# Performance work log

Hardware: AMD Instinct MI355X
Metric: run time of the kernel (lower is better)

The kernel has to match this reference:

```python
import jax, jax.numpy as jnp
import numpy as np

B = 256      # batch
ZD = 128     # z_dim
HIN = 128    # H_inputs
H = 512      # hidden
HT = 32      # H_t
N = 16384    # num nodes
RW = 16      # rw_len
TEMP = 1.0
P_DROP = 0.2
EPS_C = 0.1  # constraints epsilon


def setup_inputs() -> dict:
    key = jax.random.key(0)
    ks = jax.random.split(key, 20)
    def w(k, shape, fan):
        return (jax.random.normal(k, shape, jnp.float32) / np.float32(np.sqrt(fan)))
    z = lambda n: jnp.zeros((n,), jnp.float32)
    u = jax.random.uniform(ks[14], (RW, B, N), jnp.float32)
    return {
        "latent": jax.random.normal(ks[0], (B, ZD + 1), jnp.float32),
        "inputs0": jnp.zeros((B, HIN), jnp.float32),
        "Wc": w(ks[1], (ZD, ZD + 1), ZD + 1), "bc": z(ZD),
        "Ws": w(ks[2], (H, ZD), ZD), "bs": z(H),
        "Wh": w(ks[3], (H, H), H), "bh": z(H),
        "Wcc": w(ks[4], (H, H), H), "bcc": z(H),
        "W_ih": w(ks[5], (4 * H, HIN), HIN), "b_ih": z(4 * H),
        "W_hh": w(ks[6], (4 * H, H), H), "b_hh": z(4 * H),
        "W_up": w(ks[7], (N, H), H), "b_up": z(N),
        "W_down": w(ks[8], (HIN, N), N),
        "Wt_down": w(ks[9], (HT, H), H), "bt_down": z(HT),
        "Wt_pred": w(ks[10], (1, HT), HT),
        "Wt_up": w(ks[11], (HT, 1), 1), "bt_up": z(HT),
        "W_vt": w(ks[12], (HIN, HIN + HT), HIN + HT),
        "W_prob": w(ks[13], (1, HIN), HIN),
        # pre-sampled Gumbel noise per step (torch.rand -> gumbel)
        "gumbel": -jnp.log(-jnp.log(u + 1e-20) + 1e-20),
        # uniforms for dropout masks in TimeDecoder (forced train mode)
        "drop_u": jax.random.uniform(ks[15], (RW, B, HT), jnp.float32),
    }


def reference(latent, inputs0, Wc, bc, Ws, bs, Wh, bh, Wcc, bcc,
              W_ih, b_ih, W_hh, b_hh, W_up, b_up, W_down,
              Wt_down, bt_down, Wt_pred, Wt_up, bt_up, W_vt, W_prob,
              gumbel, drop_u):
    # induced=True path: compress latent, init (h, c)
    lat = jnp.tanh(latent @ Wc.T + bc)               # [B, ZD]
    s = jnp.tanh(lat @ Ws.T + bs)                    # [B, H]
    h0 = jnp.tanh(s @ Wh.T + bh)
    c0 = jnp.tanh(s @ Wcc.T + bcc)
    keep = 1.0 - P_DROP

    def step(carry, xs):
        x, h, c, last_t = carry
        g, du = xs
        # torch LSTMCell: gate order i, f, g, o
        gates = x @ W_ih.T + b_ih + h @ W_hh.T + b_hh  # [B, 4H]
        i, f, gg, o = jnp.split(gates, 4, axis=1)
        c2 = jax.nn.sigmoid(f) * c + jax.nn.sigmoid(i) * jnp.tanh(gg)
        h2 = jax.nn.sigmoid(o) * jnp.tanh(c2)
        # node logits + gumbel-softmax sample
        p = h2 @ W_up.T + b_up                         # [B, N]
        v = jax.nn.softmax((p + g) / TEMP, axis=1)
        Hg = v @ W_down.T                              # [B, HIN]
        # TimeDecoder (dropout always in train mode)
        td = jnp.tanh(h2 @ Wt_down.T + bt_down)        # [B, HT]
        td = td * (du < keep).astype(td.dtype) / keep
        t = jnp.minimum(td @ Wt_pred.T, 1.0)           # [B, 1]
        # constraints(t, last_t)
        mn = jnp.min(t)
        t = jnp.where(mn < EPS_C, t - mn, t)
        mx = jnp.max(t)
        t = jnp.where(mx > 1.0, t / mx, t)
        t = jnp.clip(t, last_t, 1.0)
        Ht = t @ Wt_up.T + bt_up                       # [B, HT]
        x2 = jnp.concatenate([Hg, Ht], axis=1) @ W_vt.T  # [B, HIN]
        return (x2, h2, c2, t), (v, t)

    last_t0 = jnp.zeros((latent.shape[0], 1), latent.dtype)
    (xf, _, _, _), (rw, ts) = jax.lax.scan(step, (inputs0, h0, c0, last_t0), (gumbel, drop_u))
    rw = jnp.transpose(rw, (1, 0, 2))   # [B, RW, N]
    ts = jnp.transpose(ts, (1, 0, 2))   # [B, RW, 1]
    prob = xf @ W_prob.T                # [B, 1]
    return rw, ts, prob
```

## Files before the change

kernel.cpp:

```cpp
#include <hip/hip_runtime.h>

typedef float  __attribute__((ext_vector_type(4))) f32x4;
typedef int    __attribute__((ext_vector_type(4))) i32x4;
typedef unsigned short u16;
typedef unsigned long long u64;

#define B    256
#define H    512
#define HIN  128
#define N    16384
#define RW   16
#define HT   32
#define KC2  672
#define RWN  262144
#define TS_OFF   67108864
#define PROB_OFF 67112960

__device__ __forceinline__ u16 f2bf(float f) {
  unsigned u = __builtin_bit_cast(unsigned, f);
  u += 0x7FFFu + ((u >> 16) & 1u);
  return (u16)(u >> 16);
}
__device__ __forceinline__ float bf2f(u16 v) {
  return __builtin_bit_cast(float, ((unsigned)v) << 16);
}
__device__ __forceinline__ float sigm(float x) { return 1.0f / (1.0f + expf(-x)); }

__device__ __forceinline__ void mfma(f32x4& d, i32x4 a, i32x4 b) {
  asm volatile("v_mfma_f32_16x16x32_bf16 %0, %1, %2, %0" : "+v"(d) : "v"(a), "v"(b));
}
__device__ __forceinline__ void mfma_n(f32x4& d, i32x4 a, i32x4 b) {
  asm volatile("s_nop 1\n\tv_mfma_f32_16x16x32_bf16 %0, %1, %2, %0" : "+v"(d) : "v"(a), "v"(b));
}
__device__ __forceinline__ void fence_acc(f32x4& v) {
  asm volatile("s_nop 7\n\ts_nop 7" : "+v"(v));
}

__global__ __launch_bounds__(256) void k_prep(
    const float* __restrict__ W_up, const float* __restrict__ W_down,
    const float* __restrict__ W_hh, const float* __restrict__ Wt_down,
    const float* __restrict__ b_ih, const float* __restrict__ b_hh,
    const float* __restrict__ Wh, const float* __restrict__ Wcc,
    u16* __restrict__ Wup_b, u16* __restrict__ Wdn_b, u16* __restrict__ Wfull,
    u16* __restrict__ Wtd_b, u16* __restrict__ Whc_b,
    float* __restrict__ bcomb, float* __restrict__ tstep, float* __restrict__ rowLs)
{
  const int idx0 = blockIdx.x * 256 + threadIdx.x;
  const int stride = gridDim.x * 256;
  for (int i = idx0; i < N * H; i += stride) Wup_b[i] = f2bf(W_up[i]);
  for (int i = idx0; i < HIN * N; i += stride) Wdn_b[i] = f2bf(W_down[i]);
  for (int i = idx0; i < 4 * H * H; i += stride) {
    int j = i >> 9, k = i & 511;
    Wfull[j * KC2 + 160 + k] = f2bf(W_hh[i]);
  }
  for (int i = idx0; i < HT * H; i += stride) Wtd_b[i] = f2bf(Wt_down[i]);
  for (int i = idx0; i < 2 * H * H; i += stride) {
    int j = i >> 9, k = i & 511;
    Whc_b[i] = f2bf(j < H ? Wh[j * H + k] : Wcc[(j - H) * H + k]);
  }
  for (int i = idx0; i < 4 * H; i += stride) bcomb[i] = b_ih[i] + b_hh[i];
  for (int i = idx0; i < B; i += stride) tstep[i] = 0.0f;
  for (int i = idx0; i < 16 * B; i += stride) rowLs[i] = 0.0f;
}

__global__ __launch_bounds__(256) void k_fold(
    const float* __restrict__ W_ih, const float* __restrict__ W_vt,
    const float* __restrict__ inputs0, const float* __restrict__ W_prob,
    u16* __restrict__ Wfull, float* __restrict__ g0add, float* __restrict__ wpc)
{
  int idx = blockIdx.x * 256 + threadIdx.x;
  if (idx < 2048 * 160) {
    int j = idx / 160, m = idx - j * 160;
    float a = 0.0f;
    for (int c = 0; c < HIN; ++c) a += W_ih[j * HIN + c] * W_vt[c * 160 + m];
    Wfull[j * KC2 + m] = f2bf(a);
  } else if (idx < 2048 * 160 + 256 * 2048) {
    int i2 = idx - 2048 * 160;
    int b = i2 >> 11, j = i2 & 2047;
    float a = 0.0f;
    for (int k = 0; k < HIN; ++k) a += inputs0[b * HIN + k] * W_ih[j * HIN + k];
    g0add[i2] = a;
  } else if (idx < 2048 * 160 + 256 * 2048 + 160) {
    int m = idx - (2048 * 160 + 256 * 2048);
    float a = 0.0f;
    for (int k = 0; k < HIN; ++k) a += W_prob[k] * W_vt[k * 160 + m];
    wpc[m] = a;
  }
}

__global__ __launch_bounds__(256) void k_lat(
    const float* __restrict__ latent, const float* __restrict__ Wc,
    const float* __restrict__ bc, float* __restrict__ latbuf)
{
  int idx = blockIdx.x * 256 + threadIdx.x;
  int b = idx >> 7, i = idx & 127;
  float acc = bc[i];
  for (int k = 0; k < 129; ++k) acc += latent[b * 129 + k] * Wc[i * 129 + k];
  latbuf[idx] = tanhf(acc);
}

__global__ __launch_bounds__(256) void k_sinit(
    const float* __restrict__ latbuf, const float* __restrict__ Ws,
    const float* __restrict__ bs, u16* __restrict__ sinit_b)
{
  int idx = blockIdx.x * 256 + threadIdx.x;
  int b = idx >> 9, j = idx & 511;
  float acc = bs[j];
  for (int k = 0; k < HIN; ++k) acc += latbuf[b * HIN + k] * Ws[j * HIN + k];
  sinit_b[idx] = f2bf(tanhf(acc));
}

__global__ __launch_bounds__(256) void k_h0c0m(
    const u16* __restrict__ sinit_b, const u16* __restrict__ Whc_b,
    const float* __restrict__ bh, const float* __restrict__ bcc,
    float* __restrict__ cbuf, u16* __restrict__ h0out)
{
  const int rb = blockIdx.x >> 6, cb = blockIdx.x & 63;
  const int wave = threadIdx.x >> 6, lane = threadIdx.x & 63;
  const int lr = lane & 15, lk = lane >> 4;
  const int m0 = rb * 16, col0 = cb * 16;
  const u16* ab = sinit_b + (m0 + lr) * H + wave * 128 + 8 * lk;
  const u16* bb = Whc_b + (col0 + lr) * H + wave * 128 + 8 * lk;
  f32x4 acc[2] = {};
  mfma_n(acc[0], *(const i32x4*)(ab),      *(const i32x4*)(bb));
  mfma_n(acc[1], *(const i32x4*)(ab + 32), *(const i32x4*)(bb + 32));
  mfma(acc[0], *(const i32x4*)(ab + 64), *(const i32x4*)(bb + 64));
  mfma(acc[1], *(const i32x4*)(ab + 96), *(const i32x4*)(bb + 96));
  fence_acc(acc[0]); fence_acc(acc[1]);
  __shared__ float q[4][16][17];
  #pragma unroll
  for (int rr = 0; rr < 4; ++rr)
    q[wave][4 * lk + rr][lr] = acc[0][rr] + acc[1][rr];
  __syncthreads();
  const int r2 = threadIdx.x >> 4, jj = threadIdx.x & 15;
  float s = q[0][r2][jj] + q[1][r2][jj] + q[2][r2][jj] + q[3][r2][jj];
  int col = col0 + jj;
  if (col < H) h0out[(m0 + r2) * H + col] = f2bf(tanhf(s + bh[col]));
  else         cbuf[(m0 + r2) * H + col - H] = tanhf(s + bcc[col - H]);
}

__global__ __launch_bounds__(256) void k_lstm2(
    const u16* __restrict__ hprev, u16* __restrict__ hcur,
    const u16* __restrict__ Wfull, const float* __restrict__ bcomb,
    float* __restrict__ cbuf, const float* __restrict__ g0,
    const u16* __restrict__ HgPart, const float* __restrict__ rowLs,
    const float* __restrict__ t0buf, float* __restrict__ tstep,
    const float* __restrict__ Wt_up, const float* __restrict__ bt_up,
    float* __restrict__ out, const u16* __restrict__ ebp, int r)
{
  const int blk = blockIdx.x, tid = threadIdx.x;
  const int wave = tid >> 6, lane = tid & 63;
  const int lr = lane & 15, lk = lane >> 4;
  const int rb = ((blk & 7) << 1) | ((blk >> 3) & 1);
  const int cb = blk >> 4;
  const int m0 = rb * 16, j0 = cb * 16;
  const float* rowLprev = rowLs + (r - 1) * B;

  __shared__ u16 aT[16][168];
  __shared__ float q[4][16][17];
  __shared__ float redS[8];
  __shared__ float tl[256];

  float tv = 0.0f;
  if (r > 0) {
    tv = t0buf[tid];
    float v = tv;
    #pragma unroll
    for (int off = 1; off < 64; off <<= 1) v = fminf(v, __shfl_xor(v, off));
    if (lane == 0) redS[wave] = v;
  }
  __syncthreads();
  if (r > 0) {
    float mn = fminf(fminf(redS[0], redS[1]), fminf(redS[2], redS[3]));
    if (mn < 0.1f) tv -= mn;
    float v = tv;
    #pragma unroll
    for (int off = 1; off < 64; off <<= 1) v = fmaxf(v, __shfl_xor(v, off));
    if (lane == 0) redS[4 + wave] = v;
  }
  __syncthreads();
  if (r > 0) {
    float mx = fmaxf(fmaxf(redS[4], redS[5]), fmaxf(redS[6], redS[7]));
    if (mx > 1.0f) tv /= mx;
    tv = fminf(fmaxf(tv, tstep[(r - 1) * B + tid]), 1.0f);
    if (blk == 0) {
      tstep[r * B + tid] = tv;
      out[TS_OFF + tid * RW + (r - 1)] = tv;
    }
  }
  tl[tid] = tv;

  {
    const int row = tid >> 4, c8 = (tid & 15) * 8;
    if (r > 0) {
      float s0 = 0.f, s1 = 0.f, s2 = 0.f, s3 = 0.f;
      float s4 = 0.f, s5 = 0.f, s6 = 0.f, s7 = 0.f;
      const u16* hp = HgPart + (size_t)(m0 + row) * HIN + c8;
      #pragma unroll 4
      for (int c = 0; c < 128; ++c) {
        i32x4 pk = *(const i32x4*)(hp + (size_t)c * (B * HIN));
        s0 += bf2f((u16)pk[0]); s1 += bf2f((u16)(pk[0] >> 16));
        s2 += bf2f((u16)pk[1]); s3 += bf2f((u16)(pk[1] >> 16));
        s4 += bf2f((u16)pk[2]); s5 += bf2f((u16)(pk[2] >> 16));
        s6 += bf2f((u16)pk[3]); s7 += bf2f((u16)(pk[3] >> 16));
      }
      float R = 1.0f / rowLprev[m0 + row];
      aT[row][c8 + 0] = f2bf(s0 * R); aT[row][c8 + 1] = f2bf(s1 * R);
      aT[row][c8 + 2] = f2bf(s2 * R); aT[row][c8 + 3] = f2bf(s3 * R);
      aT[row][c8 + 4] = f2bf(s4 * R); aT[row][c8 + 5] = f2bf(s5 * R);
      aT[row][c8 + 6] = f2bf(s6 * R); aT[row][c8 + 7] = f2bf(s7 * R);
    } else {
      #pragma unroll
      for (int e = 0; e < 8; ++e) aT[row][c8 + e] = 0;
    }
  }
  __syncthreads();

  for (int i2 = tid; i2 < 512; i2 += 256) {
    int row = i2 >> 5, j = i2 & 31;
    aT[row][128 + j] = (r > 0) ? f2bf(tl[m0 + row] * Wt_up[j] + bt_up[j]) : (u16)0;
  }

  if (r > 0) {
    #pragma unroll
    for (int uu = 0; uu < 8; ++uu) {
      int flat = (blk * 2048 + uu * 256 + tid) * 4;
      int row = flat >> 14;
      float Rv = 1.0f / rowLprev[row];
      u64 ev = *(const u64*)(ebp + flat);
      f32x4 o;
      o[0] = bf2f((u16)ev) * Rv;
      o[1] = bf2f((u16)(ev >> 16)) * Rv;
      o[2] = bf2f((u16)(ev >> 32)) * Rv;
      o[3] = bf2f((u16)(ev >> 48)) * Rv;
      *(f32x4*)(out + (size_t)row * RWN + (size_t)(r - 1) * N + (flat & (N - 1))) = o;
    }
  }
  __syncthreads();

  const int gcol = wave * H + j0 + lr;
  f32x4 acc[2] = {};
  const u16* brow = Wfull + (size_t)gcol * KC2 + 8 * lk;
  const u16* aL   = &aT[lr][8 * lk];
  const u16* arow = hprev + (m0 + lr) * H + 8 * lk;
  mfma_n(acc[0], *(const i32x4*)(aL),       *(const i32x4*)(brow));
  mfma_n(acc[1], *(const i32x4*)(aL + 32),  *(const i32x4*)(brow + 32));
  mfma(acc[0], *(const i32x4*)(aL + 64),  *(const i32x4*)(brow + 64));
  mfma(acc[1], *(const i32x4*)(aL + 96),  *(const i32x4*)(brow + 96));
  mfma(acc[0], *(const i32x4*)(aL + 128), *(const i32x4*)(brow + 128));
  #pragma unroll 4
  for (int i = 5; i < 21; ++i) {
    int kk = i * 32;
    mfma(acc[i & 1], *(const i32x4*)(arow + kk - 160), *(const i32x4*)(brow + kk));
  }
  fence_acc(acc[0]); fence_acc(acc[1]);
  float bias = bcomb[gcol];
  #pragma unroll
  for (int rr = 0; rr < 4; ++rr)
    q[wave][4 * lk + rr][lr] = acc[0][rr] + acc[1][rr] + bias;
  __syncthreads();
  const int r2 = tid >> 4, jj = tid & 15;
  const int b = m0 + r2, j = j0 + jj;
  float gi = q[0][r2][jj], gf = q[1][r2][jj], gg = q[2][r2][jj], go = q[3][r2][jj];
  if (r == 0) {
    const float* gp = g0 + b * 2048 + j;
    gi += gp[0]; gf += gp[512]; gg += gp[1024]; go += gp[1536];
  }
  float c  = cbuf[b * H + j];
  float c2 = sigm(gf) * c + sigm(gi) * tanhf(gg);
  float h2 = sigm(go) * tanhf(c2);
  cbuf[b * H + j] = c2;
  hcur[b * H + j] = f2bf(h2);
}

__global__ __launch_bounds__(256) void k_pgemm2(
    const u16* __restrict__ hb, const u16* __restrict__ Wup,
    const float* __restrict__ b_up, const float* __restrict__ gum,
    u16* __restrict__ eb, float* __restrict__ rowL,
    u16* __restrict__ HgPart, const u16* __restrict__ Wdn,
    const u16* __restrict__ Wtd, const float* __restrict__ bt_down,
    const float* __restrict__ Wt_pred, const float* __restrict__ du,
    float* __restrict__ t0)
{
  const int rb = blockIdx.x >> 7, cb = blockIdx.x & 127;
  const int wave = threadIdx.x >> 6, lane = threadIdx.x & 63;
  const int lr = lane & 15, lk = lane >> 4;
  const int m0 = rb * 32;
  const int n0 = cb * 128 + wave * 32;

  float gv[2][4][2], bup0 = b_up[n0 + lr], bup1 = b_up[n0 + 16 + lr];
  #pragma unroll
  for (int mi = 0; mi < 2; ++mi)
    #pragma unroll
    for (int rr = 0; rr < 4; ++rr) {
      int row = m0 + 16 * mi + 4 * lk + rr;
      gv[mi][rr][0] = gum[(size_t)row * N + n0 + lr];
      gv[mi][rr][1] = gum[(size_t)row * N + n0 + 16 + lr];
    }

  f32x4 acc[2][2] = {};
  const u16* a0 = hb + (m0 + lr) * H + 8 * lk;
  const u16* a1 = a0 + 16 * H;
  const u16* b0 = Wup + (size_t)(n0 + lr) * H + 8 * lk;
  const u16* b1 = b0 + 16 * H;
  {
    i32x4 af0 = *(const i32x4*)(a0);
    i32x4 af1 = *(const i32x4*)(a1);
    i32x4 bf0 = *(const i32x4*)(b0);
    i32x4 bf1 = *(const i32x4*)(b1);
    mfma_n(acc[0][0], af0, bf0); mfma_n(acc[0][1], af0, bf1);
    mfma_n(acc[1][0], af1, bf0); mfma_n(acc[1][1], af1, bf1);
  }
  #pragma unroll 3
  for (int kk = 32; kk < H; kk += 32) {
    i32x4 af0 = *(const i32x4*)(a0 + kk);
    i32x4 af1 = *(const i32x4*)(a1 + kk);
    i32x4 bf0 = *(const i32x4*)(b0 + kk);
    i32x4 bf1 = *(const i32x4*)(b1 + kk);
    mfma(acc[0][0], af0, bf0); mfma(acc[0][1], af0, bf1);
    mfma(acc[1][0], af1, bf0); mfma(acc[1][1], af1, bf1);
  }
  #pragma unroll
  for (int mi = 0; mi < 2; ++mi) { fence_acc(acc[mi][0]); fence_acc(acc[mi][1]); }

  __shared__ float eL[32][132];
  __shared__ float sL[4][32];
  #pragma unroll
  for (int mi = 0; mi < 2; ++mi)
    #pragma unroll
    for (int rr = 0; rr < 4; ++rr) {
      int rl = 16 * mi + 4 * lk + rr;
      int row = m0 + rl;
      u16* sp = eb + (size_t)row * N + n0 + lr;
      float v0 = acc[mi][0][rr] + bup0 + gv[mi][rr][0];
      float v1 = acc[mi][1][rr] + bup1 + gv[mi][rr][1];
      float e0 = expf(fminf(v0, 80.0f));
      float e1 = expf(fminf(v1, 80.0f));
      sp[0] = f2bf(e0); sp[16] = f2bf(e1);
      eL[rl][wave * 32 + lr] = e0;
      eL[rl][wave * 32 + 16 + lr] = e1;
      float par = e0 + e1;
      #pragma unroll
      for (int off = 1; off < 16; off <<= 1) par += __shfl_xor(par, off);
      if (lr == 0) sL[wave][rl] = par;
    }
  __syncthreads();
  if (threadIdx.x < 32)
    atomicAdd(rowL + m0 + threadIdx.x,
              sL[0][threadIdx.x] + sL[1][threadIdx.x] + sL[2][threadIdx.x] + sL[3][threadIdx.x]);

  const int nb = cb * 128;
  f32x4 acc2[2][2] = {};
  #pragma unroll
  for (int kk2 = 0; kk2 < 4; ++kk2) {
    i32x4 af[2];
    #pragma unroll
    for (int mi2 = 0; mi2 < 2; ++mi2) {
      const float* ep = &eL[16 * mi2 + lr][kk2 * 32 + 8 * lk];
      f32x4 x0 = *(const f32x4*)ep;
      f32x4 x1 = *(const f32x4*)(ep + 4);
      af[mi2][0] = (int)f2bf(x0[0]) | ((int)f2bf(x0[1]) << 16);
      af[mi2][1] = (int)f2bf(x0[2]) | ((int)f2bf(x0[3]) << 16);
      af[mi2][2] = (int)f2bf(x1[0]) | ((int)f2bf(x1[1]) << 16);
      af[mi2][3] = (int)f2bf(x1[2]) | ((int)f2bf(x1[3]) << 16);
    }
    i32x4 bf0 = *(const i32x4*)(Wdn + (size_t)(wave * 32 + lr) * N + nb + kk2 * 32 + 8 * lk);
    i32x4 bf1 = *(const i32x4*)(Wdn + (size_t)(wave * 32 + 16 + lr) * N + nb + kk2 * 32 + 8 * lk);
    mfma_n(acc2[0][0], af[0], bf0); mfma_n(acc2[0][1], af[0], bf1);
    mfma_n(acc2[1][0], af[1], bf0); mfma_n(acc2[1][1], af[1], bf1);
  }
  #pragma unroll
  for (int mi2 = 0; mi2 < 2; ++mi2) { fence_acc(acc2[mi2][0]); fence_acc(acc2[mi2][1]); }
  u16* hp = HgPart + (size_t)cb * (B * HIN);
  #pragma unroll
  for (int mi2 = 0; mi2 < 2; ++mi2)
    #pragma unroll
    for (int ni = 0; ni < 2; ++ni)
      #pragma unroll
      for (int rr = 0; rr < 4; ++rr)
        hp[(m0 + 16 * mi2 + 4 * lk + rr) * HIN + wave * 32 + 16 * ni + lr] =
            f2bf(acc2[mi2][ni][rr]);

  if (cb == 0 && wave < 2) {
    f32x4 acc3[2] = {};
    const u16* at = hb + (m0 + wave * 16 + lr) * H + 8 * lk;
    {
      i32x4 af = *(const i32x4*)(at);
      mfma_n(acc3[0], af, *(const i32x4*)(Wtd + lr * H + 8 * lk));
      mfma_n(acc3[1], af, *(const i32x4*)(Wtd + (16 + lr) * H + 8 * lk));
    }
    for (int kk = 32; kk < H; kk += 32) {
      i32x4 af = *(const i32x4*)(at + kk);
      mfma(acc3[0], af, *(const i32x4*)(Wtd + lr * H + kk + 8 * lk));
      mfma(acc3[1], af, *(const i32x4*)(Wtd + (16 + lr) * H + kk + 8 * lk));
    }
    fence_acc(acc3[0]); fence_acc(acc3[1]);
    float wp0 = Wt_pred[lr],  wp1 = Wt_pred[16 + lr];
    float bt0 = bt_down[lr],  bt1 = bt_down[16 + lr];
    #pragma unroll
    for (int rr = 0; rr < 4; ++rr) {
      int row = m0 + wave * 16 + 4 * lk + rr;
      float td0 = tanhf(acc3[0][rr] + bt0);
      float td1 = tanhf(acc3[1][rr] + bt1);
      td0 = (du[row * HT + lr]      < 0.8f) ? td0 * 1.25f : 0.0f;
      td1 = (du[row * HT + 16 + lr] < 0.8f) ? td1 * 1.25f : 0.0f;
      float part = td0 * wp0 + td1 * wp1;
      #pragma unroll
      for (int off = 1; off < 16; off <<= 1) part += __shfl_xor(part, off);
      if (lr == 0) t0[row] = fminf(part, 1.0f);
    }
  }
}

__global__ __launch_bounds__(256) void k_tail(
    float* __restrict__ out, const u16* __restrict__ eb15,
    const float* __restrict__ rowLs, const u16* __restrict__ HgPart,
    const float* __restrict__ t0buf, float* __restrict__ tstep,
    float* __restrict__ Hgf)
{
  const int blk = blockIdx.x, tid = threadIdx.x;
  const float* rowL15 = rowLs + 15 * B;
  #pragma unroll
  for (int uu = 0; uu < 4; ++uu) {
    int flat = (blk * 1024 + uu * 256 + tid) * 4;
    int row = flat >> 14;
    float Rv = 1.0f / rowL15[row];
    u64 ev = *(const u64*)(eb15 + flat);
    f32x4 o;
    o[0] = bf2f((u16)ev) * Rv;
    o[1] = bf2f((u16)(ev >> 16)) * Rv;
    o[2] = bf2f((u16)(ev >> 32)) * Rv;
    o[3] = bf2f((u16)(ev >> 48)) * Rv;
    *(f32x4*)(out + (size_t)row * RWN + (size_t)15 * N + (flat & (N - 1))) = o;
  }
  if (blk < 16) {
    const int row = blk * 16 + (tid >> 4), c8 = (tid & 15) * 8;
    float s[8] = {};
    const u16* hp = HgPart + (size_t)row * HIN + c8;
    #pragma unroll 4
    for (int c = 0; c < 128; ++c) {
      i32x4 pk = *(const i32x4*)(hp + (size_t)c * (B * HIN));
      s[0] += bf2f((u16)pk[0]); s[1] += bf2f((u16)(pk[0] >> 16));
      s[2] += bf2f((u16)pk[1]); s[3] += bf2f((u16)(pk[1] >> 16));
      s[4] += bf2f((u16)pk[2]); s[5] += bf2f((u16)(pk[2] >> 16));
      s[6] += bf2f((u16)pk[3]); s[7] += bf2f((u16)(pk[3] >> 16));
    }
    float R = 1.0f / rowL15[row];
    #pragma unroll
    for (int e = 0; e < 8; ++e) Hgf[row * HIN + c8 + e] = s[e] * R;
  }
  if (blk == 16) {
    const int wave = tid >> 6, lane = tid & 63;
    __shared__ float redS[8];
    float tv = t0buf[tid];
    float v = tv;
    #pragma unroll
    for (int off = 1; off < 64; off <<= 1) v = fminf(v, __shfl_xor(v, off));
    if (lane == 0) redS[wave] = v;
    __syncthreads();
    float mn = fminf(fminf(redS[0], redS[1]), fminf(redS[2], redS[3]));
    if (mn < 0.1f) tv -= mn;
    v = tv;
    #pragma unroll
    for (int off = 1; off < 64; off <<= 1) v = fmaxf(v, __shfl_xor(v, off));
    if (lane == 0) redS[4 + wave] = v;
    __syncthreads();
    float mx = fmaxf(fmaxf(redS[4], redS[5]), fmaxf(redS[6], redS[7]));
    if (mx > 1.0f) tv /= mx;
    tv = fminf(fmaxf(tv, tstep[15 * B + tid]), 1.0f);
    tstep[16 * B + tid] = tv;
    out[TS_OFF + tid * RW + 15] = tv;
  }
}

__global__ __launch_bounds__(256) void k_prob(
    const float* __restrict__ Hgf, const float* __restrict__ tstep,
    const float* __restrict__ Wt_up, const float* __restrict__ bt_up,
    const float* __restrict__ wpc, float* __restrict__ outp)
{
  int b = threadIdx.x;
  float acc = 0.0f;
  for (int m = 0; m < HIN; ++m) acc += Hgf[b * HIN + m] * wpc[m];
  float tv = tstep[16 * B + b];
  for (int j = 0; j < HT; ++j) acc += (tv * Wt_up[j] + bt_up[j]) * wpc[HIN + j];
  outp[b] = acc;
}

extern "C" void kernel_launch(void* const* d_in, const int* in_sizes, int n_in,
                              void* d_out, int out_size, void* d_ws, size_t ws_size,
                              hipStream_t stream) {
  (void)in_sizes; (void)n_in; (void)out_size; (void)ws_size;
  const float* latent  = (const float*)d_in[0];
  const float* inputs0 = (const float*)d_in[1];
  const float* Wc      = (const float*)d_in[2];
  const float* bc      = (const float*)d_in[3];
  const float* Ws      = (const float*)d_in[4];
  const float* bs      = (const float*)d_in[5];
  const float* Wh      = (const float*)d_in[6];
  const float* bh      = (const float*)d_in[7];
  const float* Wcc     = (const float*)d_in[8];
  const float* bcc     = (const float*)d_in[9];
  const float* W_ih    = (const float*)d_in[10];
  const float* b_ih    = (const float*)d_in[11];
  const float* W_hh    = (const float*)d_in[12];
  const float* b_hh    = (const float*)d_in[13];
  const float* W_up    = (const float*)d_in[14];
  const float* b_up    = (const float*)d_in[15];
  const float* W_down  = (const float*)d_in[16];
  const float* Wt_down = (const float*)d_in[17];
  const float* bt_down = (const float*)d_in[18];
  const float* Wt_pred = (const float*)d_in[19];
  const float* Wt_up   = (const float*)d_in[20];
  const float* bt_up   = (const float*)d_in[21];
  const float* W_vt    = (const float*)d_in[22];
  const float* W_prob  = (const float*)d_in[23];
  const float* gumbel  = (const float*)d_in[24];
  const float* drop_u  = (const float*)d_in[25];
  float* out = (float*)d_out;

  char* p = (char*)d_ws;
  auto alloc = [&](size_t bytes) { char* r = p; p += (bytes + 255) & ~(size_t)255; return r; };
  u16*   Wup_b  = (u16*)  alloc((size_t)N * H * 2);
  u16*   Wdn_b  = (u16*)  alloc((size_t)HIN * N * 2);
  u16*   Wfull_b= (u16*)  alloc((size_t)4 * H * KC2 * 2);
  u16*   Wtd_b  = (u16*)  alloc((size_t)HT * H * 2);
  u16*   Whc_b  = (u16*)  alloc((size_t)2 * H * H * 2);
  float* bcomb  = (float*)alloc(4 * H * 4);
  u16*   hbuf0  = (u16*)  alloc((size_t)B * H * 2);
  u16*   hbuf1  = (u16*)  alloc((size_t)B * H * 2);
  float* cbuf   = (float*)alloc((size_t)B * H * 4);
  u16*   sinit_b= (u16*)  alloc((size_t)B * H * 2);
  float* latbuf = (float*)alloc((size_t)B * HIN * 4);
  float* rowLs  = (float*)alloc((size_t)16 * B * 4);
  float* t0buf  = (float*)alloc(B * 4);
  float* tstep  = (float*)alloc((size_t)17 * B * 4);
  u16*   HgPart = (u16*)  alloc((size_t)128 * B * HIN * 2);
  float* Hgf    = (float*)alloc((size_t)B * HIN * 4);
  float* g0add  = (float*)alloc((size_t)B * 4 * H * 4);
  float* wpc    = (float*)alloc(160 * 4);
  u16*   ebuf0  = (u16*)  alloc((size_t)B * N * 2);
  u16*   ebuf1  = (u16*)  alloc((size_t)B * N * 2);

  k_prep<<<2048, 256, 0, stream>>>(W_up, W_down, W_hh, Wt_down, b_ih, b_hh, Wh, Wcc,
                                   Wup_b, Wdn_b, Wfull_b, Wtd_b, Whc_b, bcomb,
                                   tstep, rowLs);
  k_fold<<<3330, 256, 0, stream>>>(W_ih, W_vt, inputs0, W_prob, Wfull_b, g0add, wpc);
  k_lat  <<<128, 256, 0, stream>>>(latent, Wc, bc, latbuf);
  k_sinit<<<512, 256, 0, stream>>>(latbuf, Ws, bs, sinit_b);
  k_h0c0m<<<1024, 256, 0, stream>>>(sinit_b, Whc_b, bh, bcc, cbuf, hbuf1);

  for (int r = 0; r < 16; ++r) {
    u16* hprev = (r & 1) ? hbuf0 : hbuf1;
    u16* hcur  = (r & 1) ? hbuf1 : hbuf0;
    u16* eb    = (r & 1) ? ebuf1 : ebuf0;
    u16* ebp   = (r & 1) ? ebuf0 : ebuf1;
    k_lstm2<<<512, 256, 0, stream>>>(hprev, hcur, Wfull_b, bcomb, cbuf, g0add,
                                     HgPart, rowLs, t0buf, tstep, Wt_up, bt_up,
                                     out, ebp, r);
    k_pgemm2<<<1024, 256, 0, stream>>>(hcur, Wup_b, b_up, gumbel + (size_t)r * B * N,
                                       eb, rowLs + r * B, HgPart, Wdn_b,
                                       Wtd_b, bt_down, Wt_pred,
                                       drop_u + (size_t)r * B * HT, t0buf);
  }
  k_tail<<<1024, 256, 0, stream>>>(out, ebuf1, rowLs, HgPart, t0buf, tstep, Hgf);
  k_prob<<<1, 256, 0, stream>>>(Hgf, tstep, Wt_up, bt_up, wpc, out + PROB_OFF);
}
```

Measured before the change: 1.401 ms.

## Replace per-column-block Hg partial buffer with fp32 atomic accumulation

k_pgemm2 previously wrote 128 bf16 partial Hg tiles that k_lstm2 and k_tail then summed by reading 128 slices per element. The change accumulates the partials directly into a double-buffered fp32 Hg array with atomicAdd. The next k_lstm2 zeroes the other buffer and reads the finished sum with a single vector load. This removes the large partial-buffer traffic and the reduction loops, but adds heavy atomic contention: 128 column blocks add into each element. Summation order also becomes nondeterministic. The row-block mapping in k_lstm2 is simplified as well.

```diff
diff --git a/kernel.cpp b/kernel.cpp
--- a/kernel.cpp
+++ b/kernel.cpp
@@ -143,16 +143,16 @@
     const u16* __restrict__ hprev, u16* __restrict__ hcur,
     const u16* __restrict__ Wfull, const float* __restrict__ bcomb,
     float* __restrict__ cbuf, const float* __restrict__ g0,
-    const u16* __restrict__ HgPart, const float* __restrict__ rowLs,
-    const float* __restrict__ t0buf, float* __restrict__ tstep,
-    const float* __restrict__ Wt_up, const float* __restrict__ bt_up,
-    float* __restrict__ out, const u16* __restrict__ ebp, int r)
+    const float* __restrict__ HgfPrev, float* __restrict__ HgfNext,
+    const float* __restrict__ rowLs, const float* __restrict__ t0buf,
+    float* __restrict__ tstep, const float* __restrict__ Wt_up,
+    const float* __restrict__ bt_up, float* __restrict__ out,
+    const u16* __restrict__ ebp, int r)
 {
   const int blk = blockIdx.x, tid = threadIdx.x;
   const int wave = tid >> 6, lane = tid & 63;
   const int lr = lane & 15, lk = lane >> 4;
-  const int rb = ((blk & 7) << 1) | ((blk >> 3) & 1);
-  const int cb = blk >> 4;
+  const int rb = blk & 15, cb = blk >> 4;
   const int m0 = rb * 16, j0 = cb * 16;
   const float* rowLprev = rowLs + (r - 1) * B;
 
@@ -160,6 +160,8 @@
   __shared__ float q[4][16][17];
   __shared__ float redS[8];
   __shared__ float tl[256];
+
+  if (blk < 128) HgfNext[blk * 256 + tid] = 0.0f;
 
   float tv = 0.0f;
   if (r > 0) {
@@ -193,29 +195,21 @@
   {
     const int row = tid >> 4, c8 = (tid & 15) * 8;
     if (r > 0) {
-      float s0 = 0.f, s1 = 0.f, s2 = 0.f, s3 = 0.f;
-      float s4 = 0.f, s5 = 0.f, s6 = 0.f, s7 = 0.f;
-      const u16* hp = HgPart + (size_t)(m0 + row) * HIN + c8;
-      #pragma unroll 4
-      for (int c = 0; c < 128; ++c) {
-        i32x4 pk = *(const i32x4*)(hp + (size_t)c * (B * HIN));
-        s0 += bf2f((u16)pk[0]); s1 += bf2f((u16)(pk[0] >> 16));
-        s2 += bf2f((u16)pk[1]); s3 += bf2f((u16)(pk[1] >> 16));
-        s4 += bf2f((u16)pk[2]); s5 += bf2f((u16)(pk[2] >> 16));
-        s6 += bf2f((u16)pk[3]); s7 += bf2f((u16)(pk[3] >> 16));
-      }
+      const float* hp = HgfPrev + (m0 + row) * HIN + c8;
+      f32x4 x0 = *(const f32x4*)hp;
+      f32x4 x1 = *(const f32x4*)(hp + 4);
       float R = 1.0f / rowLprev[m0 + row];
-      aT[row][c8 + 0] = f2bf(s0 * R); aT[row][c8 + 1] = f2bf(s1 * R);
-      aT[row][c8 + 2] = f2bf(s2 * R); aT[row][c8 + 3] = f2bf(s3 * R);
-      aT[row][c8 + 4] = f2bf(s4 * R); aT[row][c8 + 5] = f2bf(s5 * R);
-      aT[row][c8 + 6] = f2bf(s6 * R); aT[row][c8 + 7] = f2bf(s7 * R);
+      aT[row][c8 + 0] = f2bf(x0[0] * R); aT[row][c8 + 1] = f2bf(x0[1] * R);
+      aT[row][c8 + 2] = f2bf(x0[2] * R); aT[row][c8 + 3] = f2bf(x0[3] * R);
+      aT[row][c8 + 4] = f2bf(x1[0] * R); aT[row][c8 + 5] = f2bf(x1[1] * R);
+      aT[row][c8 + 6] = f2bf(x1[2] * R); aT[row][c8 + 7] = f2bf(x1[3] * R);
     } else {
       #pragma unroll
       for (int e = 0; e < 8; ++e) aT[row][c8 + e] = 0;
     }
   }
-  __syncthreads();
-
+
+  __syncthreads();
   for (int i2 = tid; i2 < 512; i2 += 256) {
     int row = i2 >> 5, j = i2 & 31;
     aT[row][128 + j] = (r > 0) ? f2bf(tl[m0 + row] * Wt_up[j] + bt_up[j]) : (u16)0;
@@ -277,7 +271,7 @@
     const u16* __restrict__ hb, const u16* __restrict__ Wup,
     const float* __restrict__ b_up, const float* __restrict__ gum,
     u16* __restrict__ eb, float* __restrict__ rowL,
-    u16* __restrict__ HgPart, const u16* __restrict__ Wdn,
+    float* __restrict__ HgfAcc, const u16* __restrict__ Wdn,
     const u16* __restrict__ Wtd, const float* __restrict__ bt_down,
     const float* __restrict__ Wt_pred, const float* __restrict__ du,
     float* __restrict__ t0)
@@ -371,15 +365,14 @@
   }
   #pragma unroll
   for (int mi2 = 0; mi2 < 2; ++mi2) { fence_acc(acc2[mi2][0]); fence_acc(acc2[mi2][1]); }
-  u16* hp = HgPart + (size_t)cb * (B * HIN);
   #pragma unroll
   for (int mi2 = 0; mi2 < 2; ++mi2)
     #pragma unroll
     for (int ni = 0; ni < 2; ++ni)
       #pragma unroll
       for (int rr = 0; rr < 4; ++rr)
-        hp[(m0 + 16 * mi2 + 4 * lk + rr) * HIN + wave * 32 + 16 * ni + lr] =
-            f2bf(acc2[mi2][ni][rr]);
+        atomicAdd(HgfAcc + (m0 + 16 * mi2 + 4 * lk + rr) * HIN + wave * 32 + 16 * ni + lr,
+                  acc2[mi2][ni][rr]);
 
   if (cb == 0 && wave < 2) {
     f32x4 acc3[2] = {};
@@ -414,9 +407,8 @@
 
 __global__ __launch_bounds__(256) void k_tail(
     float* __restrict__ out, const u16* __restrict__ eb15,
-    const float* __restrict__ rowLs, const u16* __restrict__ HgPart,
-    const float* __restrict__ t0buf, float* __restrict__ tstep,
-    float* __restrict__ Hgf)
+    const float* __restrict__ rowLs, const float* __restrict__ t0buf,
+    float* __restrict__ tstep)
 {
   const int blk = blockIdx.x, tid = threadIdx.x;
   const float* rowL15 = rowLs + 15 * B;
@@ -433,23 +425,7 @@
     o[3] = bf2f((u16)(ev >> 48)) * Rv;
     *(f32x4*)(out + (size_t)row * RWN + (size_t)15 * N + (flat & (N - 1))) = o;
   }
-  if (blk < 16) {
-    const int row = blk * 16 + (tid >> 4), c8 = (tid & 15) * 8;
-    float s[8] = {};
-    const u16* hp = HgPart + (size_t)row * HIN + c8;
-    #pragma unroll 4
-    for (int c = 0; c < 128; ++c) {
-      i32x4 pk = *(const i32x4*)(hp + (size_t)c * (B * HIN));
-      s[0] += bf2f((u16)pk[0]); s[1] += bf2f((u16)(pk[0] >> 16));
-      s[2] += bf2f((u16)pk[1]); s[3] += bf2f((u16)(pk[1] >> 16));
-      s[4] += bf2f((u16)pk[2]); s[5] += bf2f((u16)(pk[2] >> 16));
-      s[6] += bf2f((u16)pk[3]); s[7] += bf2f((u16)(pk[3] >> 16));
-    }
-    float R = 1.0f / rowL15[row];
-    #pragma unroll
-    for (int e = 0; e < 8; ++e) Hgf[row * HIN + c8 + e] = s[e] * R;
-  }
-  if (blk == 16) {
+  if (blk == 0) {
     const int wave = tid >> 6, lane = tid & 63;
     __shared__ float redS[8];
     float tv = t0buf[tid];
@@ -474,13 +450,15 @@
 }
 
 __global__ __launch_bounds__(256) void k_prob(
-    const float* __restrict__ Hgf, const float* __restrict__ tstep,
-    const float* __restrict__ Wt_up, const float* __restrict__ bt_up,
-    const float* __restrict__ wpc, float* __restrict__ outp)
+    const float* __restrict__ Hgf15, const float* __restrict__ rowLs,
+    const float* __restrict__ tstep, const float* __restrict__ Wt_up,
+    const float* __restrict__ bt_up, const float* __restrict__ wpc,
+    float* __restrict__ outp)
 {
   int b = threadIdx.x;
+  float R = 1.0f / rowLs[15 * B + b];
   float acc = 0.0f;
-  for (int m = 0; m < HIN; ++m) acc += Hgf[b * HIN + m] * wpc[m];
+  for (int m = 0; m < HIN; ++m) acc += Hgf15[b * HIN + m] * R * wpc[m];
   float tv = tstep[16 * B + b];
   for (int j = 0; j < HT; ++j) acc += (tv * Wt_up[j] + bt_up[j]) * wpc[HIN + j];
   outp[b] = acc;
@@ -534,8 +512,8 @@
   float* rowLs  = (float*)alloc((size_t)16 * B * 4);
   float* t0buf  = (float*)alloc(B * 4);
   float* tstep  = (float*)alloc((size_t)17 * B * 4);
-  u16*   HgPart = (u16*)  alloc((size_t)128 * B * HIN * 2);
-  float* Hgf    = (float*)alloc((size_t)B * HIN * 4);
+  float* Hgf2_0 = (float*)alloc((size_t)B * HIN * 4);
+  float* Hgf2_1 = (float*)alloc((size_t)B * HIN * 4);
   float* g0add  = (float*)alloc((size_t)B * 4 * H * 4);
   float* wpc    = (float*)alloc(160 * 4);
   u16*   ebuf0  = (u16*)  alloc((size_t)B * N * 2);
@@ -554,14 +532,16 @@
     u16* hcur  = (r & 1) ? hbuf1 : hbuf0;
     u16* eb    = (r & 1) ? ebuf1 : ebuf0;
     u16* ebp   = (r & 1) ? ebuf0 : ebuf1;
+    float* HgfCur  = (r & 1) ? Hgf2_1 : Hgf2_0;
+    float* HgfPrev = (r & 1) ? Hgf2_0 : Hgf2_1;
     k_lstm2<<<512, 256, 0, stream>>>(hprev, hcur, Wfull_b, bcomb, cbuf, g0add,
-                                     HgPart, rowLs, t0buf, tstep, Wt_up, bt_up,
-                                     out, ebp, r);
+                                     HgfPrev, HgfCur, rowLs, t0buf, tstep,
+                                     Wt_up, bt_up, out, ebp, r);
     k_pgemm2<<<1024, 256, 0, stream>>>(hcur, Wup_b, b_up, gumbel + (size_t)r * B * N,
-                                       eb, rowLs + r * B, HgPart, Wdn_b,
+                                       eb, rowLs + r * B, HgfCur, Wdn_b,
                                        Wtd_b, bt_down, Wt_pred,
                                        drop_u + (size_t)r * B * HT, t0buf);
   }
-  k_tail<<<1024, 256, 0, stream>>>(out, ebuf1, rowLs, HgPart, t0buf, tstep, Hgf);
-  k_prob<<<1, 256, 0, stream>>>(Hgf, tstep, Wt_up, bt_up, wpc, out + PROB_OFF);
-}
+  k_tail<<<1024, 256, 0, stream>>>(out, ebuf1, rowLs, t0buf, tstep);
+  k_prob<<<1, 256, 0, stream>>>(Hgf2_1, rowLs, tstep, Wt_up, bt_up, wpc, out + PROB_OFF);
+}
```

Result: faster. 1.293 ms (-7.7%).
